# Kernel tuning notes

Measured on AMD Instinct MI355X. Metric: run time of the kernel, lower is better.

## Reference

```python
import jax, jax.numpy as jnp
import numpy as np

NEG_SLOPE = 0.01  # torch nn.LeakyReLU default

def _lrelu(x):
    return jnp.where(x >= 0, x, NEG_SLOPE * x)

def setup_inputs() -> dict:
    key = jax.random.key(0)
    ks = jax.random.split(key, 10)
    B, Din, C = 128, 2048, 2048
    H = C // 2            # 1024
    OUT, KD = C // 4, 20  # 512, 20 (MBD)
    s = lambda k, shape, fan: jax.random.normal(k, shape, jnp.float32) / np.sqrt(fan)
    return {
        "inputs": jax.random.normal(ks[0], (B, Din), jnp.float32),
        "W1": s(ks[1], (Din, C), Din), "b1": jnp.zeros((C,), jnp.float32),
        "W2": s(ks[2], (C, H), C),     "b2": jnp.zeros((H,), jnp.float32),
        "W3": s(ks[3], (H, H), H),     "b3": jnp.zeros((H,), jnp.float32),
        "T":  jax.random.normal(ks[4], (H, OUT, KD), jnp.float32),
        "Wc": s(ks[5], (H + OUT, 1), H + OUT), "bc": jnp.zeros((1,), jnp.float32),
    }

def reference(inputs, W1, b1, W2, b2, W3, b3, T, Wc, bc):
    # dense stack: Linear + LeakyReLU x3
    h = _lrelu(inputs @ W1 + b1)          # [B, 2048]
    h = _lrelu(h @ W2 + b2)               # [B, 1024]
    h = _lrelu(h @ W3 + b3)               # [B, 1024]
    # minibatch discrimination
    Hd, OUT, KD = T.shape
    M = (h @ T.reshape(Hd, OUT * KD)).reshape(-1, OUT, KD)   # [B, OUT, KD]
    # pairwise L1 over kernel dim: [B, B, OUT]
    norm = jnp.abs(M[None, :, :, :] - M[:, None, :, :]).sum(-1)
    o_b = jnp.exp(-norm).sum(0) - 1.0     # [B, OUT] (subtract self-term)
    feat = jnp.concatenate([h, o_b], axis=1)  # [B, 1536]
    return feat @ Wc + bc                 # [B, 1]
```

## Files before the change

### kernel.cpp

```cpp
#include <hip/hip_runtime.h>
#include <hip/hip_bf16.h>


typedef __bf16 bf16x8 __attribute__((ext_vector_type(8)));
typedef __bf16 bf16x2 __attribute__((ext_vector_type(2)));
typedef float  f32x4  __attribute__((ext_vector_type(4)));

#define OFF_H1HI 8388608
#define OFF_H1LO 8912896
#define OFF_H2HI 9437184
#define OFF_H2LO 9699328
#define OFF_H3HI 9961472
#define OFF_FEAT 10223616

static __device__ __forceinline__ unsigned int f2bf(float f) {
  union { float f; unsigned int u; } v; v.f = f;
  unsigned int r = v.u + 0x7FFFu + ((v.u >> 16) & 1u);
  return r >> 16;
}
static __device__ __forceinline__ float bf2f(unsigned short u) {
  union { unsigned int u; float f; } v; v.u = ((unsigned int)u) << 16;
  return v.f;
}
static __device__ __forceinline__ unsigned int pack_bf16_rne(float a, float b) {
  bf16x2 v; v[0] = (__bf16)a; v[1] = (__bf16)b;
  return __builtin_bit_cast(unsigned int, v);
}
static __device__ __forceinline__ float lrelu(float x) {
  return x >= 0.0f ? x : 0.01f * x;
}
static __device__ __forceinline__ void split8(const float* x, uint4& h, uint4& l) {
  unsigned* hp = (unsigned*)&h; unsigned* lp = (unsigned*)&l;
  #pragma unroll
  for (int i = 0; i < 4; i++) {
    float x0 = x[2 * i], x1 = x[2 * i + 1];
    unsigned hu = pack_bf16_rne(x0, x1);
    float f0 = bf2f((unsigned short)(hu & 0xFFFFu));
    float f1 = bf2f((unsigned short)(hu >> 16));
    hp[i] = hu;
    lp[i] = pack_bf16_rne(x0 - f0, x1 - f1);
  }
}

__global__ __launch_bounds__(256, 2) void k_gemm1(
    const float* __restrict__ X, const float* __restrict__ W,
    float* __restrict__ P)
{
  __shared__ __align__(16) char smem[30720];
  unsigned short* AHs = (unsigned short*)smem;
  unsigned short* ALs = (unsigned short*)(smem + 10240);
  unsigned int*   WHs = (unsigned int*)(smem + 20480);
  unsigned int*   WLs = (unsigned int*)(smem + 25600);
  const int t     = threadIdx.x;
  const int c0    = blockIdx.x * 64;
  const int kbase = blockIdx.y * 256;
  const int lane  = t & 63, wave = t >> 6;
  const int ml    = lane & 15, q = lane >> 4;
  const int r0    = wave * 32;
  const int ra = t >> 2, qa = t & 3;
  const int kp = t & 15, n4 = (t >> 4) * 4;

  f32x4 acc[2][4];
  #pragma unroll
  for (int i = 0; i < 2; i++)
    #pragma unroll
    for (int j = 0; j < 4; j++) acc[i][j] = (f32x4){0.f, 0.f, 0.f, 0.f};

  const float* xp0 = X + (size_t)ra * 2048 + kbase + qa * 8;
  const float* xp1 = xp0 + (size_t)64 * 2048;
  const float* wp  = W + (size_t)(kbase + 2 * kp) * 2048 + c0 + n4;
  float xr0[8], xr1[8];
  *(float4*)(xr0 + 0) = *(const float4*)xp0;
  *(float4*)(xr0 + 4) = *(const float4*)(xp0 + 4);
  *(float4*)(xr1 + 0) = *(const float4*)xp1;
  *(float4*)(xr1 + 4) = *(const float4*)(xp1 + 4);
  float4 vw0 = *(const float4*)wp;
  float4 vw1 = *(const float4*)(wp + 2048);

  for (int kt = 0; kt < 8; kt++) {
    uint4 h0, l0, h1, l1;
    split8(xr0, h0, l0); split8(xr1, h1, l1);
    *(uint4*)(AHs + ra * 40 + qa * 8)        = h0;
    *(uint4*)(AHs + (ra + 64) * 40 + qa * 8) = h1;
    *(uint4*)(ALs + ra * 40 + qa * 8)        = l0;
    *(uint4*)(ALs + (ra + 64) * 40 + qa * 8) = l1;
    {
      float w0[4], w1[4];
      *(float4*)w0 = vw0; *(float4*)w1 = vw1;
      #pragma unroll
      for (int c = 0; c < 4; c++) {
        unsigned int hu = pack_bf16_rne(w0[c], w1[c]);
        float f0 = bf2f((unsigned short)(hu & 0xFFFFu));
        float f1 = bf2f((unsigned short)(hu >> 16));
        unsigned int lu = pack_bf16_rne(w0[c] - f0, w1[c] - f1);
        WHs[(n4 + c) * 20 + kp] = hu;
        WLs[(n4 + c) * 20 + kp] = lu;
      }
    }
    __syncthreads();
    if (kt < 7) {
      xp0 += 32; xp1 += 32;
      wp  += (size_t)32 * 2048;
      *(float4*)(xr0 + 0) = *(const float4*)xp0;
      *(float4*)(xr0 + 4) = *(const float4*)(xp0 + 4);
      *(float4*)(xr1 + 0) = *(const float4*)xp1;
      *(float4*)(xr1 + 4) = *(const float4*)(xp1 + 4);
      vw0 = *(const float4*)wp;
      vw1 = *(const float4*)(wp + 2048);
    }
    bf16x8 ah0 = *(const bf16x8*)(AHs + (r0 + ml) * 40 + q * 8);
    bf16x8 ah1 = *(const bf16x8*)(AHs + (r0 + 16 + ml) * 40 + q * 8);
    bf16x8 al0 = *(const bf16x8*)(ALs + (r0 + ml) * 40 + q * 8);
    bf16x8 al1 = *(const bf16x8*)(ALs + (r0 + 16 + ml) * 40 + q * 8);
    #pragma unroll
    for (int ct = 0; ct < 4; ct++) {
      bf16x8 bh = *(const bf16x8*)((const unsigned short*)WHs +
                                   (size_t)((ct * 16 + ml) * 20 + q * 4) * 2);
      bf16x8 bl = *(const bf16x8*)((const unsigned short*)WLs +
                                   (size_t)((ct * 16 + ml) * 20 + q * 4) * 2);
      acc[0][ct] = __builtin_amdgcn_mfma_f32_16x16x32_bf16(ah0, bh, acc[0][ct], 0, 0, 0);
      acc[1][ct] = __builtin_amdgcn_mfma_f32_16x16x32_bf16(ah1, bh, acc[1][ct], 0, 0, 0);
      acc[0][ct] = __builtin_amdgcn_mfma_f32_16x16x32_bf16(ah0, bl, acc[0][ct], 0, 0, 0);
      acc[1][ct] = __builtin_amdgcn_mfma_f32_16x16x32_bf16(ah1, bl, acc[1][ct], 0, 0, 0);
      acc[0][ct] = __builtin_amdgcn_mfma_f32_16x16x32_bf16(al0, bh, acc[0][ct], 0, 0, 0);
      acc[1][ct] = __builtin_amdgcn_mfma_f32_16x16x32_bf16(al1, bh, acc[1][ct], 0, 0, 0);
    }
    __syncthreads();
  }

  float* op = P + (size_t)blockIdx.y * 128 * 2048;
  #pragma unroll
  for (int rt = 0; rt < 2; rt++)
    #pragma unroll
    for (int ct = 0; ct < 4; ct++) {
      const int col = c0 + ct * 16 + ml;
      const int row = r0 + rt * 16 + q * 4;
      #pragma unroll
      for (int i = 0; i < 4; i++)
        op[(size_t)(row + i) * 2048 + col] = acc[rt][ct][i];
    }
}

__global__ __launch_bounds__(256, 2) void k_gemm3(
    const unsigned short* __restrict__ Ahi, const unsigned short* __restrict__ Alo,
    const float* __restrict__ W, float* __restrict__ P,
    int K, int N, int kchunk)
{
  __shared__ __align__(16) char smem[30720];
  unsigned short* AHs = (unsigned short*)smem;
  unsigned short* ALs = (unsigned short*)(smem + 10240);
  unsigned int*   WHs = (unsigned int*)(smem + 20480);
  unsigned int*   WLs = (unsigned int*)(smem + 25600);
  const int t     = threadIdx.x;
  const int c0    = blockIdx.x * 64;
  const int kbase = blockIdx.y * kchunk;
  const int lane  = t & 63, wave = t >> 6;
  const int ml    = lane & 15, q = lane >> 4;
  const int r0    = wave * 32;
  const int ra = t >> 2, qa = t & 3;
  const int kp = t & 15, n4 = (t >> 4) * 4;

  f32x4 acc[2][4];
  #pragma unroll
  for (int i = 0; i < 2; i++)
    #pragma unroll
    for (int j = 0; j < 4; j++) acc[i][j] = (f32x4){0.f, 0.f, 0.f, 0.f};

  const unsigned short* ahp = Ahi + (size_t)ra * K + kbase + qa * 8;
  const unsigned short* alp = Alo + (size_t)ra * K + kbase + qa * 8;
  const float*          wp  = W + (size_t)(kbase + 2 * kp) * N + c0 + n4;
  uint4  vah0 = *(const uint4*)ahp;
  uint4  vah1 = *(const uint4*)(ahp + (size_t)64 * K);
  uint4  val0 = *(const uint4*)alp;
  uint4  val1 = *(const uint4*)(alp + (size_t)64 * K);
  float4 vw0 = *(const float4*)wp;
  float4 vw1 = *(const float4*)(wp + N);

  const int nkt = kchunk >> 5;
  for (int kt = 0; kt < nkt; kt++) {
    *(uint4*)(AHs + ra * 40 + qa * 8)        = vah0;
    *(uint4*)(AHs + (ra + 64) * 40 + qa * 8) = vah1;
    *(uint4*)(ALs + ra * 40 + qa * 8)        = val0;
    *(uint4*)(ALs + (ra + 64) * 40 + qa * 8) = val1;
    {
      float w0[4], w1[4];
      *(float4*)w0 = vw0; *(float4*)w1 = vw1;
      #pragma unroll
      for (int c = 0; c < 4; c++) {
        unsigned int hu = pack_bf16_rne(w0[c], w1[c]);
        float f0 = bf2f((unsigned short)(hu & 0xFFFFu));
        float f1 = bf2f((unsigned short)(hu >> 16));
        unsigned int lu = pack_bf16_rne(w0[c] - f0, w1[c] - f1);
        WHs[(n4 + c) * 20 + kp] = hu;
        WLs[(n4 + c) * 20 + kp] = lu;
      }
    }
    __syncthreads();
    if (kt + 1 < nkt) {
      ahp += 32; alp += 32;
      wp  += (size_t)32 * N;
      vah0 = *(const uint4*)ahp;
      vah1 = *(const uint4*)(ahp + (size_t)64 * K);
      val0 = *(const uint4*)alp;
      val1 = *(const uint4*)(alp + (size_t)64 * K);
      vw0 = *(const float4*)wp;
      vw1 = *(const float4*)(wp + N);
    }
    bf16x8 ah0 = *(const bf16x8*)(AHs + (r0 + ml) * 40 + q * 8);
    bf16x8 ah1 = *(const bf16x8*)(AHs + (r0 + 16 + ml) * 40 + q * 8);
    bf16x8 al0 = *(const bf16x8*)(ALs + (r0 + ml) * 40 + q * 8);
    bf16x8 al1 = *(const bf16x8*)(ALs + (r0 + 16 + ml) * 40 + q * 8);
    #pragma unroll
    for (int ct = 0; ct < 4; ct++) {
      bf16x8 bh = *(const bf16x8*)((const unsigned short*)WHs +
                                   (size_t)((ct * 16 + ml) * 20 + q * 4) * 2);
      bf16x8 bl = *(const bf16x8*)((const unsigned short*)WLs +
                                   (size_t)((ct * 16 + ml) * 20 + q * 4) * 2);
      acc[0][ct] = __builtin_amdgcn_mfma_f32_16x16x32_bf16(ah0, bh, acc[0][ct], 0, 0, 0);
      acc[1][ct] = __builtin_amdgcn_mfma_f32_16x16x32_bf16(ah1, bh, acc[1][ct], 0, 0, 0);
      acc[0][ct] = __builtin_amdgcn_mfma_f32_16x16x32_bf16(ah0, bl, acc[0][ct], 0, 0, 0);
      acc[1][ct] = __builtin_amdgcn_mfma_f32_16x16x32_bf16(ah1, bl, acc[1][ct], 0, 0, 0);
      acc[0][ct] = __builtin_amdgcn_mfma_f32_16x16x32_bf16(al0, bh, acc[0][ct], 0, 0, 0);
      acc[1][ct] = __builtin_amdgcn_mfma_f32_16x16x32_bf16(al1, bh, acc[1][ct], 0, 0, 0);
    }
    __syncthreads();
  }

  float* op = P + (size_t)blockIdx.y * 128 * N;
  #pragma unroll
  for (int rt = 0; rt < 2; rt++)
    #pragma unroll
    for (int ct = 0; ct < 4; ct++) {
      const int col = c0 + ct * 16 + ml;
      const int row = r0 + rt * 16 + q * 4;
      #pragma unroll
      for (int i = 0; i < 4; i++)
        op[(size_t)(row + i) * N + col] = acc[rt][ct][i];
    }
}

__global__ __launch_bounds__(256) void k_reduce(
    const float* __restrict__ P, const float* __restrict__ bias,
    float* __restrict__ outF, unsigned short* __restrict__ outHi,
    unsigned short* __restrict__ outLo, int N, int S, int ldo)
{
  const int gid = blockIdx.x * 256 + threadIdx.x;
  const int c4 = N >> 2;
  if (gid >= 128 * c4) return;
  const int r = gid / c4;
  const int c = (gid - r * c4) * 4;
  float4 s = make_float4(0, 0, 0, 0);
  for (int si = 0; si < S; si++) {
    float4 p = *(const float4*)(P + (size_t)si * 128 * N + (size_t)r * N + c);
    s.x += p.x; s.y += p.y; s.z += p.z; s.w += p.w;
  }
  float4 b = *(const float4*)(bias + c);
  s.x = lrelu(s.x + b.x); s.y = lrelu(s.y + b.y);
  s.z = lrelu(s.z + b.z); s.w = lrelu(s.w + b.w);
  if (outF) *(float4*)(outF + (size_t)r * ldo + c) = s;
  if (outHi) {
    ushort4 uh;
    uh.x = (unsigned short)f2bf(s.x); uh.y = (unsigned short)f2bf(s.y);
    uh.z = (unsigned short)f2bf(s.z); uh.w = (unsigned short)f2bf(s.w);
    *(ushort4*)(outHi + (size_t)r * N + c) = uh;
    if (outLo) {
      ushort4 ul;
      ul.x = (unsigned short)f2bf(s.x - bf2f(uh.x));
      ul.y = (unsigned short)f2bf(s.y - bf2f(uh.y));
      ul.z = (unsigned short)f2bf(s.z - bf2f(uh.z));
      ul.w = (unsigned short)f2bf(s.w - bf2f(uh.w));
      *(ushort4*)(outLo + (size_t)r * N + c) = ul;
    }
  }
}

__global__ __launch_bounds__(256, 2) void k_gemm4(
    const unsigned short* __restrict__ h3b, const float* __restrict__ T,
    unsigned short* __restrict__ accM)
{
  __shared__ __align__(16) char smem[15360];
  unsigned short* Asm = (unsigned short*)smem;
  unsigned int*   Wst = (unsigned int*)(smem + 10240);
  const int t    = threadIdx.x;
  const int c0   = blockIdx.x * 64;
  const int lane = t & 63, wave = t >> 6;
  const int ml   = lane & 15, q = lane >> 4;
  const int r0   = wave * 32;
  const int ra = t >> 2, qa = t & 3;
  const int kp = t & 15, n4 = (t >> 4) * 4;

  f32x4 acc[2][4];
  #pragma unroll
  for (int i = 0; i < 2; i++)
    #pragma unroll
    for (int j = 0; j < 4; j++) acc[i][j] = (f32x4){0.f, 0.f, 0.f, 0.f};

  const unsigned short* ap = h3b + (size_t)ra * 1024 + qa * 8;
  const float*          tp = T + (size_t)(2 * kp) * 10240 + c0 + n4;
  uint4  va0 = *(const uint4*)ap;
  uint4  va1 = *(const uint4*)(ap + 64 * 1024);
  float4 vw0 = *(const float4*)tp;
  float4 vw1 = *(const float4*)(tp + 10240);

  for (int kt = 0; kt < 32; kt++) {
    *(uint4*)(Asm + ra * 40 + qa * 8)        = va0;
    *(uint4*)(Asm + (ra + 64) * 40 + qa * 8) = va1;
    Wst[(n4 + 0) * 20 + kp] = f2bf(vw0.x) | (f2bf(vw1.x) << 16);
    Wst[(n4 + 1) * 20 + kp] = f2bf(vw0.y) | (f2bf(vw1.y) << 16);
    Wst[(n4 + 2) * 20 + kp] = f2bf(vw0.z) | (f2bf(vw1.z) << 16);
    Wst[(n4 + 3) * 20 + kp] = f2bf(vw0.w) | (f2bf(vw1.w) << 16);
    __syncthreads();
    if (kt < 31) {
      ap += 32;
      tp += (size_t)32 * 10240;
      va0 = *(const uint4*)ap;
      va1 = *(const uint4*)(ap + 64 * 1024);
      vw0 = *(const float4*)tp;
      vw1 = *(const float4*)(tp + 10240);
    }
    bf16x8 a0 = *(const bf16x8*)(Asm + (r0 + ml) * 40 + q * 8);
    bf16x8 a1 = *(const bf16x8*)(Asm + (r0 + 16 + ml) * 40 + q * 8);
    #pragma unroll
    for (int ct = 0; ct < 4; ct++) {
      bf16x8 b = *(const bf16x8*)((const unsigned short*)Wst +
                                  (size_t)((ct * 16 + ml) * 20 + q * 4) * 2);
      acc[0][ct] = __builtin_amdgcn_mfma_f32_16x16x32_bf16(a0, b, acc[0][ct], 0, 0, 0);
      acc[1][ct] = __builtin_amdgcn_mfma_f32_16x16x32_bf16(a1, b, acc[1][ct], 0, 0, 0);
    }
    __syncthreads();
  }

  #pragma unroll
  for (int rt = 0; rt < 2; rt++)
    #pragma unroll
    for (int ct = 0; ct < 4; ct++) {
      int col = c0 + ct * 16 + ml;
      int row = r0 + rt * 16 + q * 4;
      #pragma unroll
      for (int i = 0; i < 4; i++)
        accM[(size_t)(row + i) * 10240 + col] = (unsigned short)f2bf(acc[rt][ct][i]);
    }
}

__global__ __launch_bounds__(256, 4) void k_pairwise(
    const unsigned short* __restrict__ accM, float* __restrict__ feat)
{
  __shared__ __align__(16) char smem[12288];
  float* Ml    = (float*)smem;
  float* parts = (float*)(smem + 10240);
  const int t = threadIdx.x;
  const int o = blockIdx.x;
  {
    int i = t >> 1, kh = (t & 1) * 10;
    const unsigned short* p = accM + (size_t)i * 10240 + o * 20 + kh;
    #pragma unroll
    for (int k = 0; k < 10; k++) Ml[i * 20 + kh + k] = bf2f(p[k]);
  }
  __syncthreads();

  const int jg = t & 63, strip = t >> 6;
  float mj[2][20];
  #pragma unroll
  for (int c = 0; c < 2; c++) {
    const float* src = Ml + (size_t)(jg * 2 + c) * 20;
    #pragma unroll
    for (int k = 0; k < 20; k++) mj[c][k] = src[k];
  }
  float acc2[2] = {0.f, 0.f};
  for (int ii = 0; ii < 32; ii++) {
    int i = strip * 32 + ii;
    const float4* m4 = (const float4*)(Ml + (size_t)i * 20);
    float mi[20];
    *(float4*)(mi + 0)  = m4[0]; *(float4*)(mi + 4)  = m4[1];
    *(float4*)(mi + 8)  = m4[2]; *(float4*)(mi + 12) = m4[3];
    *(float4*)(mi + 16) = m4[4];
    #pragma unroll
    for (int c = 0; c < 2; c++) {
      float norm = 0.f;
      #pragma unroll
      for (int k = 0; k < 20; k++) norm += fabsf(mi[k] - mj[c][k]);
      acc2[c] += __expf(-norm);
    }
  }
  parts[strip * 128 + jg * 2 + 0] = acc2[0];
  parts[strip * 128 + jg * 2 + 1] = acc2[1];
  __syncthreads();
  if (t < 128) {
    float s = parts[t] + parts[128 + t] + parts[256 + t] + parts[384 + t];
    feat[(size_t)t * 1536 + 1024 + o] = s - 1.0f;
  }
}

__global__ __launch_bounds__(256) void k_final(
    const float* __restrict__ feat, const float* __restrict__ Wc,
    const float* __restrict__ bc, float* __restrict__ out)
{
  __shared__ float red[4];
  const int t = threadIdx.x, r = blockIdx.x;
  float s = 0.f;
  for (int c = t; c < 1536; c += 256) s += feat[(size_t)r * 1536 + c] * Wc[c];
  for (int off = 32; off > 0; off >>= 1) s += __shfl_down(s, off);
  if ((t & 63) == 0) red[t >> 6] = s;
  __syncthreads();
  if (t == 0) out[r] = red[0] + red[1] + red[2] + red[3] + bc[0];
}

extern "C" void kernel_launch(void* const* d_in, const int* in_sizes, int n_in,
                              void* d_out, int out_size, void* d_ws, size_t ws_size,
                              hipStream_t stream)
{
  const float* X  = (const float*)d_in[0];
  const float* W1 = (const float*)d_in[1];
  const float* b1 = (const float*)d_in[2];
  const float* W2 = (const float*)d_in[3];
  const float* b2 = (const float*)d_in[4];
  const float* W3 = (const float*)d_in[5];
  const float* b3 = (const float*)d_in[6];
  const float* T  = (const float*)d_in[7];
  const float* Wc = (const float*)d_in[8];
  const float* bc = (const float*)d_in[9];

  char* ws = (char*)d_ws;
  float*          P    = (float*)ws;
  unsigned short* accM = (unsigned short*)ws;
  unsigned short* h1hi = (unsigned short*)(ws + OFF_H1HI);
  unsigned short* h1lo = (unsigned short*)(ws + OFF_H1LO);
  unsigned short* h2hi = (unsigned short*)(ws + OFF_H2HI);
  unsigned short* h2lo = (unsigned short*)(ws + OFF_H2LO);
  unsigned short* h3hi = (unsigned short*)(ws + OFF_H3HI);
  float*          feat = (float*)(ws + OFF_FEAT);
  float*          out  = (float*)d_out;

  k_gemm1<<<dim3(32, 8), 256, 0, stream>>>(X, W1, P);
  k_reduce<<<256, 256, 0, stream>>>(P, b1, nullptr, h1hi, h1lo, 2048, 8, 0);
  k_gemm3<<<dim3(16, 16), 256, 0, stream>>>(h1hi, h1lo, W2, P, 2048, 1024, 128);
  k_reduce<<<128, 256, 0, stream>>>(P, b2, nullptr, h2hi, h2lo, 1024, 16, 0);
  k_gemm3<<<dim3(16, 8), 256, 0, stream>>>(h2hi, h2lo, W3, P, 1024, 1024, 128);
  k_reduce<<<128, 256, 0, stream>>>(P, b3, feat, h3hi, nullptr, 1024, 8, 1536);
  k_gemm4<<<160, 256, 0, stream>>>(h3hi, T, accM);
  k_pairwise<<<512, 256, 0, stream>>>(accM, feat);
  k_final<<<128, 256, 0, stream>>>(feat, Wc, bc, out);
}
```

Baseline: 190.7 us.

## Split-K the MBD GEMM and fuse the final linear into reduce and pairwise

Splits the h3·T GEMM into two K halves across a second grid dimension so more CUs stream the large T tensor, writing two bf16 partials. The pairwise kernel sums the partials, uses 512 threads, and adds its weighted contribution directly to the output with atomics. The last reduce kernel computes the h·Wc dot product and bias, removing the feat buffer and the final kernel. The partials are rounded to bf16 before summing, which adds a bit of rounding error.

```diff
diff --git a/kernel.cpp b/kernel.cpp
--- a/kernel.cpp
+++ b/kernel.cpp
@@ -11,7 +11,6 @@
 #define OFF_H2HI 9437184
 #define OFF_H2LO 9699328
 #define OFF_H3HI 9961472
-#define OFF_FEAT 10223616
 
 static __device__ __forceinline__ unsigned int f2bf(float f) {
   union { float f; unsigned int u; } v; v.f = f;
@@ -241,8 +240,8 @@
 
 __global__ __launch_bounds__(256) void k_reduce(
     const float* __restrict__ P, const float* __restrict__ bias,
-    float* __restrict__ outF, unsigned short* __restrict__ outHi,
-    unsigned short* __restrict__ outLo, int N, int S, int ldo)
+    unsigned short* __restrict__ outHi, unsigned short* __restrict__ outLo,
+    int N, int S)
 {
   const int gid = blockIdx.x * 256 + threadIdx.x;
   const int c4 = N >> 2;
@@ -257,21 +256,45 @@
   float4 b = *(const float4*)(bias + c);
   s.x = lrelu(s.x + b.x); s.y = lrelu(s.y + b.y);
   s.z = lrelu(s.z + b.z); s.w = lrelu(s.w + b.w);
-  if (outF) *(float4*)(outF + (size_t)r * ldo + c) = s;
-  if (outHi) {
-    ushort4 uh;
-    uh.x = (unsigned short)f2bf(s.x); uh.y = (unsigned short)f2bf(s.y);
-    uh.z = (unsigned short)f2bf(s.z); uh.w = (unsigned short)f2bf(s.w);
-    *(ushort4*)(outHi + (size_t)r * N + c) = uh;
-    if (outLo) {
-      ushort4 ul;
-      ul.x = (unsigned short)f2bf(s.x - bf2f(uh.x));
-      ul.y = (unsigned short)f2bf(s.y - bf2f(uh.y));
-      ul.z = (unsigned short)f2bf(s.z - bf2f(uh.z));
-      ul.w = (unsigned short)f2bf(s.w - bf2f(uh.w));
-      *(ushort4*)(outLo + (size_t)r * N + c) = ul;
-    }
-  }
+  ushort4 uh;
+  uh.x = (unsigned short)f2bf(s.x); uh.y = (unsigned short)f2bf(s.y);
+  uh.z = (unsigned short)f2bf(s.z); uh.w = (unsigned short)f2bf(s.w);
+  *(ushort4*)(outHi + (size_t)r * N + c) = uh;
+  ushort4 ul;
+  ul.x = (unsigned short)f2bf(s.x - bf2f(uh.x));
+  ul.y = (unsigned short)f2bf(s.y - bf2f(uh.y));
+  ul.z = (unsigned short)f2bf(s.z - bf2f(uh.z));
+  ul.w = (unsigned short)f2bf(s.w - bf2f(uh.w));
+  *(ushort4*)(outLo + (size_t)r * N + c) = ul;
+}
+
+__global__ __launch_bounds__(256) void k_reduce3(
+    const float* __restrict__ P, const float* __restrict__ bias,
+    const float* __restrict__ Wc, const float* __restrict__ bc,
+    unsigned short* __restrict__ outHi, float* __restrict__ out)
+{
+  __shared__ float red[4];
+  const int t = threadIdx.x, r = blockIdx.x;
+  const int c = t * 4;
+  float4 s = make_float4(0, 0, 0, 0);
+  for (int si = 0; si < 8; si++) {
+    float4 p = *(const float4*)(P + (size_t)si * 128 * 1024 + (size_t)r * 1024 + c);
+    s.x += p.x; s.y += p.y; s.z += p.z; s.w += p.w;
+  }
+  float4 b = *(const float4*)(bias + c);
+  s.x = lrelu(s.x + b.x); s.y = lrelu(s.y + b.y);
+  s.z = lrelu(s.z + b.z); s.w = lrelu(s.w + b.w);
+  ushort4 uh;
+  uh.x = (unsigned short)f2bf(s.x); uh.y = (unsigned short)f2bf(s.y);
+  uh.z = (unsigned short)f2bf(s.z); uh.w = (unsigned short)f2bf(s.w);
+  *(ushort4*)(outHi + (size_t)r * 1024 + c) = uh;
+
+  float4 w = *(const float4*)(Wc + c);
+  float d = s.x * w.x + s.y * w.y + s.z * w.z + s.w * w.w;
+  for (int off = 32; off > 0; off >>= 1) d += __shfl_down(d, off);
+  if ((t & 63) == 0) red[t >> 6] = d;
+  __syncthreads();
+  if (t == 0) out[r] = red[0] + red[1] + red[2] + red[3] + bc[0];
 }
 
 __global__ __launch_bounds__(256, 2) void k_gemm4(
@@ -281,8 +304,9 @@
   __shared__ __align__(16) char smem[15360];
   unsigned short* Asm = (unsigned short*)smem;
   unsigned int*   Wst = (unsigned int*)(smem + 10240);
-  const int t    = threadIdx.x;
-  const int c0   = blockIdx.x * 64;
+  const int t     = threadIdx.x;
+  const int c0    = blockIdx.x * 64;
+  const int kbase = blockIdx.y * 512;
   const int lane = t & 63, wave = t >> 6;
   const int ml   = lane & 15, q = lane >> 4;
   const int r0   = wave * 32;
@@ -295,14 +319,14 @@
     #pragma unroll
     for (int j = 0; j < 4; j++) acc[i][j] = (f32x4){0.f, 0.f, 0.f, 0.f};
 
-  const unsigned short* ap = h3b + (size_t)ra * 1024 + qa * 8;
-  const float*          tp = T + (size_t)(2 * kp) * 10240 + c0 + n4;
+  const unsigned short* ap = h3b + (size_t)ra * 1024 + kbase + qa * 8;
+  const float*          tp = T + (size_t)(kbase + 2 * kp) * 10240 + c0 + n4;
   uint4  va0 = *(const uint4*)ap;
   uint4  va1 = *(const uint4*)(ap + 64 * 1024);
   float4 vw0 = *(const float4*)tp;
   float4 vw1 = *(const float4*)(tp + 10240);
 
-  for (int kt = 0; kt < 32; kt++) {
+  for (int kt = 0; kt < 16; kt++) {
     *(uint4*)(Asm + ra * 40 + qa * 8)        = va0;
     *(uint4*)(Asm + (ra + 64) * 40 + qa * 8) = va1;
     Wst[(n4 + 0) * 20 + kp] = f2bf(vw0.x) | (f2bf(vw1.x) << 16);
@@ -310,7 +334,7 @@
     Wst[(n4 + 2) * 20 + kp] = f2bf(vw0.z) | (f2bf(vw1.z) << 16);
     Wst[(n4 + 3) * 20 + kp] = f2bf(vw0.w) | (f2bf(vw1.w) << 16);
     __syncthreads();
-    if (kt < 31) {
+    if (kt < 15) {
       ap += 32;
       tp += (size_t)32 * 10240;
       va0 = *(const uint4*)ap;
@@ -330,6 +354,7 @@
     __syncthreads();
   }
 
+  unsigned short* outp = accM + (size_t)blockIdx.y * 1310720;
   #pragma unroll
   for (int rt = 0; rt < 2; rt++)
     #pragma unroll
@@ -338,27 +363,29 @@
       int row = r0 + rt * 16 + q * 4;
       #pragma unroll
       for (int i = 0; i < 4; i++)
-        accM[(size_t)(row + i) * 10240 + col] = (unsigned short)f2bf(acc[rt][ct][i]);
-    }
-}
-
-__global__ __launch_bounds__(256, 4) void k_pairwise(
-    const unsigned short* __restrict__ accM, float* __restrict__ feat)
-{
-  __shared__ __align__(16) char smem[12288];
-  float* Ml    = (float*)smem;
-  float* parts = (float*)(smem + 10240);
+        outp[(size_t)(row + i) * 10240 + col] = (unsigned short)f2bf(acc[rt][ct][i]);
+    }
+}
+
+__global__ __launch_bounds__(512, 4) void k_pairwise(
+    const unsigned short* __restrict__ accM, const float* __restrict__ Wc,
+    float* __restrict__ out)
+{
+  __shared__ __align__(16) float Ml[128 * 20];
+  __shared__ float parts[8 * 128];
   const int t = threadIdx.x;
   const int o = blockIdx.x;
+  const float wco = Wc[1024 + o];
   {
-    int i = t >> 1, kh = (t & 1) * 10;
+    int i = t >> 2, kh = (t & 3) * 5;
     const unsigned short* p = accM + (size_t)i * 10240 + o * 20 + kh;
     #pragma unroll
-    for (int k = 0; k < 10; k++) Ml[i * 20 + kh + k] = bf2f(p[k]);
+    for (int k = 0; k < 5; k++)
+      Ml[i * 20 + kh + k] = bf2f(p[k]) + bf2f(p[1310720 + k]);
   }
   __syncthreads();
 
-  const int jg = t & 63, strip = t >> 6;
+  const int jg = t & 63, ihalf = t >> 6;
   float mj[2][20];
   #pragma unroll
   for (int c = 0; c < 2; c++) {
@@ -367,8 +394,8 @@
     for (int k = 0; k < 20; k++) mj[c][k] = src[k];
   }
   float acc2[2] = {0.f, 0.f};
-  for (int ii = 0; ii < 32; ii++) {
-    int i = strip * 32 + ii;
+  for (int ii = 0; ii < 16; ii++) {
+    int i = ihalf * 16 + ii;
     const float4* m4 = (const float4*)(Ml + (size_t)i * 20);
     float mi[20];
     *(float4*)(mi + 0)  = m4[0]; *(float4*)(mi + 4)  = m4[1];
@@ -382,27 +409,15 @@
       acc2[c] += __expf(-norm);
     }
   }
-  parts[strip * 128 + jg * 2 + 0] = acc2[0];
-  parts[strip * 128 + jg * 2 + 1] = acc2[1];
+  parts[ihalf * 128 + jg * 2 + 0] = acc2[0];
+  parts[ihalf * 128 + jg * 2 + 1] = acc2[1];
   __syncthreads();
   if (t < 128) {
-    float s = parts[t] + parts[128 + t] + parts[256 + t] + parts[384 + t];
-    feat[(size_t)t * 1536 + 1024 + o] = s - 1.0f;
-  }
-}
-
-__global__ __launch_bounds__(256) void k_final(
-    const float* __restrict__ feat, const float* __restrict__ Wc,
-    const float* __restrict__ bc, float* __restrict__ out)
-{
-  __shared__ float red[4];
-  const int t = threadIdx.x, r = blockIdx.x;
-  float s = 0.f;
-  for (int c = t; c < 1536; c += 256) s += feat[(size_t)r * 1536 + c] * Wc[c];
-  for (int off = 32; off > 0; off >>= 1) s += __shfl_down(s, off);
-  if ((t & 63) == 0) red[t >> 6] = s;
-  __syncthreads();
-  if (t == 0) out[r] = red[0] + red[1] + red[2] + red[3] + bc[0];
+    float s = 0.f;
+    #pragma unroll
+    for (int ih = 0; ih < 8; ih++) s += parts[ih * 128 + t];
+    atomicAdd(&out[t], (s - 1.0f) * wco);
+  }
 }
 
 extern "C" void kernel_launch(void* const* d_in, const int* in_sizes, int n_in,
@@ -428,16 +443,14 @@
   unsigned short* h2hi = (unsigned short*)(ws + OFF_H2HI);
   unsigned short* h2lo = (unsigned short*)(ws + OFF_H2LO);
   unsigned short* h3hi = (unsigned short*)(ws + OFF_H3HI);
-  float*          feat = (float*)(ws + OFF_FEAT);
   float*          out  = (float*)d_out;
 
   k_gemm1<<<dim3(32, 8), 256, 0, stream>>>(X, W1, P);
-  k_reduce<<<256, 256, 0, stream>>>(P, b1, nullptr, h1hi, h1lo, 2048, 8, 0);
+  k_reduce<<<256, 256, 0, stream>>>(P, b1, h1hi, h1lo, 2048, 8);
   k_gemm3<<<dim3(16, 16), 256, 0, stream>>>(h1hi, h1lo, W2, P, 2048, 1024, 128);
-  k_reduce<<<128, 256, 0, stream>>>(P, b2, nullptr, h2hi, h2lo, 1024, 16, 0);
+  k_reduce<<<128, 256, 0, stream>>>(P, b2, h2hi, h2lo, 1024, 16);
   k_gemm3<<<dim3(16, 8), 256, 0, stream>>>(h2hi, h2lo, W3, P, 1024, 1024, 128);
-  k_reduce<<<128, 256, 0, stream>>>(P, b3, feat, h3hi, nullptr, 1024, 8, 1536);
-  k_gemm4<<<160, 256, 0, stream>>>(h3hi, T, accM);
-  k_pairwise<<<512, 256, 0, stream>>>(accM, feat);
-  k_final<<<128, 256, 0, stream>>>(feat, Wc, bc, out);
-}
+  k_reduce3<<<128, 256, 0, stream>>>(P, b3, Wc, bc, h3hi, out);
+  k_gemm4<<<dim3(160, 2), 256, 0, stream>>>(h3hi, T, accM);
+  k_pairwise<<<512, 512, 0, stream>>>(accM, Wc, out);
+}
```

New measurement: 182.3 us. 1.05x faster.
